# Kernel tuning notes

Measured on AMD Instinct MI355X. Metric: run time of the kernel, lower is better.

Reference implementation:

```python
import jax, jax.numpy as jnp
import numpy as np

B, N = 1, 2048
C_REF, C_ATOM, C_PAIR = 389, 128, 16


def setup_inputs() -> dict:
    key = jax.random.key(0)
    ks = jax.random.split(key, 12)
    inp = {
        "ref_pos": jax.random.normal(ks[0], (B, N, 3), jnp.float32),
        "ref_charge": jax.random.normal(ks[1], (B, N), jnp.float32),
        "ref_mask": jnp.ones((B, N), jnp.float32),
        "ref_element": jax.random.uniform(ks[2], (B, N, 128), jnp.float32),
        "ref_atom_name_chars": jax.random.uniform(ks[3], (B, N, 4, 64), jnp.float32),
        "ref_space_uid": jax.random.randint(ks[4], (B, N), 0, 256, jnp.int32),
        # learned params (fan-in scaled init)
        "W_feats": jax.random.normal(ks[5], (C_REF, C_ATOM), jnp.float32) / np.sqrt(C_REF),
        "b_feats": jnp.zeros((C_ATOM,), jnp.float32),
        "W_off": jax.random.normal(ks[6], (3, C_PAIR), jnp.float32) / np.sqrt(3.0),
        "b_off": jnp.zeros((C_PAIR,), jnp.float32),
        "W_inv": jax.random.normal(ks[7], (1, C_PAIR), jnp.float32),
        "b_inv": jnp.zeros((C_PAIR,), jnp.float32),
        "W_vm": jax.random.normal(ks[8], (1, C_PAIR), jnp.float32),
        "b_vm": jnp.zeros((C_PAIR,), jnp.float32),
    }
    return inp


def reference(ref_pos, ref_charge, ref_mask, ref_element, ref_atom_name_chars,
              ref_space_uid, W_feats, b_feats, W_off, b_off, W_inv, b_inv,
              W_vm, b_vm):
    # --- atom single conditioning cl: [B, N, c_atom] ---
    names_flat = ref_atom_name_chars.reshape(*ref_atom_name_chars.shape[:-2], -1)  # [B,N,256]
    feats = jnp.concatenate(
        [ref_pos, ref_charge[..., None], ref_mask[..., None], ref_element, names_flat],
        axis=-1)  # [B,N,389]
    cl = feats @ W_feats + b_feats

    # --- atom pair conditioning plm: [B, N, N, c_atom_pair] ---
    dlm = ref_pos[..., :, None, :] - ref_pos[..., None, :, :]  # [B,N,N,3]
    vlm = (ref_space_uid[..., None, :] == ref_space_uid[..., :, None]).astype(dlm.dtype)  # [B,N,N]
    v = vlm[..., None]  # [B,N,N,1]

    plm = (dlm @ W_off + b_off) * v
    inv_sq = 1.0 / (1.0 + jnp.sum(dlm * dlm, axis=-1, keepdims=True))  # [B,N,N,1]
    plm = plm + (inv_sq @ W_inv + b_inv) * v
    plm = plm + (v @ W_vm + b_vm) * v
    return cl, plm
```

## Files before the change

### kernel.cpp

```cpp
#include <hip/hip_runtime.h>

#define NN 2048
#define CA 128
#define CR 389
#define CP 16

typedef float nfloat4 __attribute__((ext_vector_type(4)));

__global__ __launch_bounds__(1024) void cl_kernel(
    const float* __restrict__ pos, const float* __restrict__ charge,
    const float* __restrict__ mask, const float* __restrict__ elem,
    const float* __restrict__ names, const float* __restrict__ Wf,
    const float* __restrict__ bfeats, float* __restrict__ cl)
{
    __shared__ float ft[8][CR];
    const int tid = threadIdx.x;
    const int n0 = blockIdx.x * 8;

    for (int idx = tid; idx < 8 * CR; idx += 1024) {
        int a = idx / CR;
        int k = idx - a * CR;
        int n = n0 + a;
        float v;
        if (k < 3)         v = pos[n * 3 + k];
        else if (k == 3)   v = charge[n];
        else if (k == 4)   v = mask[n];
        else if (k < 133)  v = elem[n * 128 + (k - 5)];
        else               v = names[n * 256 + (k - 133)];
        ft[a][k] = v;
    }
    __syncthreads();

    const int c = tid & 127;
    const int a = tid >> 7;
    const float* fa = ft[a];
    float acc = 0.f;
    #pragma unroll 8
    for (int k = 0; k < CR; ++k)
        acc = fmaf(fa[k], Wf[k * CA + c], acc);

    __builtin_nontemporal_store(acc + bfeats[c], &cl[(size_t)(n0 + a) * CA + c]);
}

__global__ __launch_bounds__(256) void plm_kernel(
    const float* __restrict__ pos, const int* __restrict__ uid,
    const float* __restrict__ Woff, const float* __restrict__ boff,
    const float* __restrict__ Winv, const float* __restrict__ binv,
    const float* __restrict__ Wvm, const float* __restrict__ bvm,
    float* __restrict__ out)
{
    const int tid = threadIdx.x;
    const int q = tid & 3;
    const int p = tid >> 2;

    float w0[4], w1[4], w2[4], wi[4], kk[4];
    #pragma unroll
    for (int i = 0; i < 4; ++i) {
        int c = q * 4 + i;
        w0[i] = Woff[c];
        w1[i] = Woff[CP + c];
        w2[i] = Woff[2 * CP + c];
        wi[i] = Winv[c];
        kk[i] = Wvm[c] + boff[c] + binv[c] + bvm[c];
    }

    const int l = blockIdx.x;
    const float plx = pos[l * 3 + 0];
    const float ply = pos[l * 3 + 1];
    const float plz = pos[l * 3 + 2];
    const int ul = uid[l];
    nfloat4* __restrict__ dst = (nfloat4*)(out + (size_t)l * NN * CP);

    #pragma unroll 4
    for (int j = 0; j < NN / 64; ++j) {
        const int m = j * 64 + p;
        const float dx = plx - pos[m * 3 + 0];
        const float dy = ply - pos[m * 3 + 1];
        const float dz = plz - pos[m * 3 + 2];
        const float inv = 1.0f / (1.0f + dx * dx + dy * dy + dz * dz);
        const unsigned sel = (uid[m] == ul) ? 0xFFFFFFFFu : 0u;

        float rx = fmaf(dx, w0[0], fmaf(dy, w1[0], fmaf(dz, w2[0], fmaf(inv, wi[0], kk[0]))));
        float ry = fmaf(dx, w0[1], fmaf(dy, w1[1], fmaf(dz, w2[1], fmaf(inv, wi[1], kk[1]))));
        float rz = fmaf(dx, w0[2], fmaf(dy, w1[2], fmaf(dz, w2[2], fmaf(inv, wi[2], kk[2]))));
        float rw = fmaf(dx, w0[3], fmaf(dy, w1[3], fmaf(dz, w2[3], fmaf(inv, wi[3], kk[3]))));

        unsigned ux = __float_as_uint(rx) & sel;
        unsigned uy = __float_as_uint(ry) & sel;
        unsigned uz = __float_as_uint(rz) & sel;
        unsigned uw = __float_as_uint(rw) & sel;

        nfloat4 r;
        r.x = __uint_as_float(ux);
        r.y = __uint_as_float(uy);
        r.z = __uint_as_float(uz);
        r.w = __uint_as_float(uw);

        __builtin_nontemporal_store(r, dst + j * 256 + tid);
    }
}

extern "C" void kernel_launch(void* const* d_in, const int* in_sizes, int n_in,
                              void* d_out, int out_size, void* d_ws, size_t ws_size,
                              hipStream_t stream)
{
    const float* pos    = (const float*)d_in[0];
    const float* charge = (const float*)d_in[1];
    const float* mask   = (const float*)d_in[2];
    const float* elem   = (const float*)d_in[3];
    const float* names  = (const float*)d_in[4];
    const int*   uid    = (const int*)  d_in[5];
    const float* Wf     = (const float*)d_in[6];
    const float* bfeats = (const float*)d_in[7];
    const float* Woff   = (const float*)d_in[8];
    const float* boff   = (const float*)d_in[9];
    const float* Winv   = (const float*)d_in[10];
    const float* binv   = (const float*)d_in[11];
    const float* Wvm    = (const float*)d_in[12];
    const float* bvm    = (const float*)d_in[13];

    float* cl  = (float*)d_out;
    float* plm = (float*)d_out + (size_t)NN * CA;

    cl_kernel<<<NN / 8, 1024, 0, stream>>>(pos, charge, mask, elem, names, Wf, bfeats, cl);
    plm_kernel<<<NN, 256, 0, stream>>>(pos, uid, Woff, boff, Winv, binv, Wvm, bvm, plm);
}
```

Baseline: 337.0 us.

## Fuse cl and plm kernels into one launch with block-range dispatch

```diff
diff --git a/kernel.cpp b/kernel.cpp
--- a/kernel.cpp
+++ b/kernel.cpp
@@ -5,98 +5,98 @@
 #define CR 389
 #define CP 16
 
-typedef float nfloat4 __attribute__((ext_vector_type(4)));
-
-__global__ __launch_bounds__(1024) void cl_kernel(
+__global__ __launch_bounds__(256) void fused_kernel(
     const float* __restrict__ pos, const float* __restrict__ charge,
     const float* __restrict__ mask, const float* __restrict__ elem,
     const float* __restrict__ names, const float* __restrict__ Wf,
-    const float* __restrict__ bfeats, float* __restrict__ cl)
+    const float* __restrict__ bfeats,
+    const int* __restrict__ uid,
+    const float* __restrict__ Woff, const float* __restrict__ boff,
+    const float* __restrict__ Winv, const float* __restrict__ binv,
+    const float* __restrict__ Wvm, const float* __restrict__ bvm,
+    float* __restrict__ cl, float* __restrict__ plm)
 {
     __shared__ float ft[8][CR];
     const int tid = threadIdx.x;
-    const int n0 = blockIdx.x * 8;
 
-    for (int idx = tid; idx < 8 * CR; idx += 1024) {
-        int a = idx / CR;
-        int k = idx - a * CR;
-        int n = n0 + a;
-        float v;
-        if (k < 3)         v = pos[n * 3 + k];
-        else if (k == 3)   v = charge[n];
-        else if (k == 4)   v = mask[n];
-        else if (k < 133)  v = elem[n * 128 + (k - 5)];
-        else               v = names[n * 256 + (k - 133)];
-        ft[a][k] = v;
-    }
-    __syncthreads();
+    if (blockIdx.x < NN) {
+        const int q = tid & 3;
+        const int p = tid >> 2;
 
-    const int c = tid & 127;
-    const int a = tid >> 7;
-    const float* fa = ft[a];
-    float acc = 0.f;
-    #pragma unroll 8
-    for (int k = 0; k < CR; ++k)
-        acc = fmaf(fa[k], Wf[k * CA + c], acc);
+        float w0[4], w1[4], w2[4], wi[4], kk[4];
+        #pragma unroll
+        for (int i = 0; i < 4; ++i) {
+            int c = q * 4 + i;
+            w0[i] = Woff[c];
+            w1[i] = Woff[CP + c];
+            w2[i] = Woff[2 * CP + c];
+            wi[i] = Winv[c];
+            kk[i] = Wvm[c] + boff[c] + binv[c] + bvm[c];
+        }
 
-    __builtin_nontemporal_store(acc + bfeats[c], &cl[(size_t)(n0 + a) * CA + c]);
-}
+        const int l = blockIdx.x;
+        const float plx = pos[l * 3 + 0];
+        const float ply = pos[l * 3 + 1];
+        const float plz = pos[l * 3 + 2];
+        const int ul = uid[l];
+        float4* __restrict__ dst = (float4*)(plm + (size_t)l * NN * CP);
 
-__global__ __launch_bounds__(256) void plm_kernel(
-    const float* __restrict__ pos, const int* __restrict__ uid,
-    const float* __restrict__ Woff, const float* __restrict__ boff,
-    const float* __restrict__ Winv, const float* __restrict__ binv,
-    const float* __restrict__ Wvm, const float* __restrict__ bvm,
-    float* __restrict__ out)
-{
-    const int tid = threadIdx.x;
-    const int q = tid & 3;
-    const int p = tid >> 2;
+        #pragma unroll 4
+        for (int j = 0; j < NN / 64; ++j) {
+            const int m = j * 64 + p;
+            const float dx = plx - pos[m * 3 + 0];
+            const float dy = ply - pos[m * 3 + 1];
+            const float dz = plz - pos[m * 3 + 2];
+            const float inv = 1.0f / (1.0f + dx * dx + dy * dy + dz * dz);
+            const unsigned sel = (uid[m] == ul) ? 0xFFFFFFFFu : 0u;
 
-    float w0[4], w1[4], w2[4], wi[4], kk[4];
-    #pragma unroll
-    for (int i = 0; i < 4; ++i) {
-        int c = q * 4 + i;
-        w0[i] = Woff[c];
-        w1[i] = Woff[CP + c];
-        w2[i] = Woff[2 * CP + c];
-        wi[i] = Winv[c];
-        kk[i] = Wvm[c] + boff[c] + binv[c] + bvm[c];
-    }
+            float rx = fmaf(dx, w0[0], fmaf(dy, w1[0], fmaf(dz, w2[0], fmaf(inv, wi[0], kk[0]))));
+            float ry = fmaf(dx, w0[1], fmaf(dy, w1[1], fmaf(dz, w2[1], fmaf(inv, wi[1], kk[1]))));
+            float rz = fmaf(dx, w0[2], fmaf(dy, w1[2], fmaf(dz, w2[2], fmaf(inv, wi[2], kk[2]))));
+            float rw = fmaf(dx, w0[3], fmaf(dy, w1[3], fmaf(dz, w2[3], fmaf(inv, wi[3], kk[3]))));
 
-    const int l = blockIdx.x;
-    const float plx = pos[l * 3 + 0];
-    const float ply = pos[l * 3 + 1];
-    const float plz = pos[l * 3 + 2];
-    const int ul = uid[l];
-    nfloat4* __restrict__ dst = (nfloat4*)(out + (size_t)l * NN * CP);
+            float4 r;
+            r.x = __uint_as_float(__float_as_uint(rx) & sel);
+            r.y = __uint_as_float(__float_as_uint(ry) & sel);
+            r.z = __uint_as_float(__float_as_uint(rz) & sel);
+            r.w = __uint_as_float(__float_as_uint(rw) & sel);
 
-    #pragma unroll 4
-    for (int j = 0; j < NN / 64; ++j) {
-        const int m = j * 64 + p;
-        const float dx = plx - pos[m * 3 + 0];
-        const float dy = ply - pos[m * 3 + 1];
-        const float dz = plz - pos[m * 3 + 2];
-        const float inv = 1.0f / (1.0f + dx * dx + dy * dy + dz * dz);
-        const unsigned sel = (uid[m] == ul) ? 0xFFFFFFFFu : 0u;
+            dst[j * 256 + tid] = r;
+        }
+    } else {
+        const int n0 = (blockIdx.x - NN) * 8;
 
-        float rx = fmaf(dx, w0[0], fmaf(dy, w1[0], fmaf(dz, w2[0], fmaf(inv, wi[0], kk[0]))));
-        float ry = fmaf(dx, w0[1], fmaf(dy, w1[1], fmaf(dz, w2[1], fmaf(inv, wi[1], kk[1]))));
-        float rz = fmaf(dx, w0[2], fmaf(dy, w1[2], fmaf(dz, w2[2], fmaf(inv, wi[2], kk[2]))));
-        float rw = fmaf(dx, w0[3], fmaf(dy, w1[3], fmaf(dz, w2[3], fmaf(inv, wi[3], kk[3]))));
+        for (int idx = tid; idx < 8 * CR; idx += 256) {
+            int a = idx / CR;
+            int k = idx - a * CR;
+            int n = n0 + a;
+            float v;
+            if (k < 3)         v = pos[n * 3 + k];
+            else if (k == 3)   v = charge[n];
+            else if (k == 4)   v = mask[n];
+            else if (k < 133)  v = elem[n * 128 + (k - 5)];
+            else               v = names[n * 256 + (k - 133)];
+            ft[a][k] = v;
+        }
+        __syncthreads();
 
-        unsigned ux = __float_as_uint(rx) & sel;
-        unsigned uy = __float_as_uint(ry) & sel;
-        unsigned uz = __float_as_uint(rz) & sel;
-        unsigned uw = __float_as_uint(rw) & sel;
-
-        nfloat4 r;
-        r.x = __uint_as_float(ux);
-        r.y = __uint_as_float(uy);
-        r.z = __uint_as_float(uz);
-        r.w = __uint_as_float(uw);
-
-        __builtin_nontemporal_store(r, dst + j * 256 + tid);
+        const int c = tid & 127;
+        const int half = tid >> 7;
+        float a0 = 0.f, a1 = 0.f, a2 = 0.f, a3 = 0.f;
+        #pragma unroll 4
+        for (int k = 0; k < CR; ++k) {
+            const float w = Wf[k * CA + c];
+            a0 = fmaf(ft[half * 4 + 0][k], w, a0);
+            a1 = fmaf(ft[half * 4 + 1][k], w, a1);
+            a2 = fmaf(ft[half * 4 + 2][k], w, a2);
+            a3 = fmaf(ft[half * 4 + 3][k], w, a3);
+        }
+        const float bb = bfeats[c];
+        const int nb = n0 + half * 4;
+        cl[(size_t)(nb + 0) * CA + c] = a0 + bb;
+        cl[(size_t)(nb + 1) * CA + c] = a1 + bb;
+        cl[(size_t)(nb + 2) * CA + c] = a2 + bb;
+        cl[(size_t)(nb + 3) * CA + c] = a3 + bb;
     }
 }
 
@@ -122,6 +122,7 @@
     float* cl  = (float*)d_out;
     float* plm = (float*)d_out + (size_t)NN * CA;
 
-    cl_kernel<<<NN / 8, 1024, 0, stream>>>(pos, charge, mask, elem, names, Wf, bfeats, cl);
-    plm_kernel<<<NN, 256, 0, stream>>>(pos, uid, Woff, boff, Winv, binv, Wvm, bvm, plm);
+    fused_kernel<<<NN + NN / 8, 256, 0, stream>>>(
+        pos, charge, mask, elem, names, Wf, bfeats, uid,
+        Woff, boff, Winv, binv, Wvm, bvm, cl, plm);
 }
```

Result: slower. 364.4 us (+8.1%).
